# Kernel optimization log

Measured on AMD Instinct MI355X. Metric: run time of the kernel, lower is better.

## Reference

```python
import jax, jax.numpy as jnp
import numpy as np

N_SIDE = 8
N_PATCHES = 24
W_NORMALS = 1.0
W_PLANAR = 1.0
W_COLLISION = 0.01
W_TEMPLATE = 1.0
W_SYMMETRY = 0.0
SIGMA = 0.1

_lin = np.linspace(0.0, 1.0, N_SIDE).astype(np.float32)
_S, _T = np.meshgrid(_lin, _lin, indexing='ij')
S_GRID = jnp.asarray(_S.flatten())
T_GRID = jnp.asarray(_T.flatten())

def _build_topology():
    n = N_SIDE
    tris = []
    for i in range(n - 1):
        for j in range(n - 1):
            v00 = i * n + j; v10 = (i + 1) * n + j
            v01 = i * n + j + 1; v11 = (i + 1) * n + j + 1
            tris.append([v00, v10, v01]); tris.append([v10, v11, v01])
    tris = np.array(tris, dtype=np.int32)
    edges_pts = np.array([
        [i * n + 0 for i in range(n)],        # edge 0: t=0
        [(n - 1) * n + j for j in range(n)],  # edge 1: s=1
        [i * n + (n - 1) for i in range(n)],  # edge 2: t=1
        [0 * n + j for j in range(n)],        # edge 3: s=0
    ], dtype=np.int32)
    edges_tris = []
    for e in edges_pts:
        es = set(int(x) for x in e)
        et = [ti for ti, t in enumerate(tris) if len(es.intersection(int(v) for v in t)) >= 2]
        edges_tris.append(et[: n - 1])
    return tris, edges_pts, np.array(edges_tris, dtype=np.int32)

TRIANGULATION, GRID_POINT_EDGES, TRIANGULATION_EDGES = _build_topology()

ADJ_PAIRS = [(i, (i + 1) % N_PATCHES, 1) for i in range(N_PATCHES)]
_adjset = set(tuple(sorted((i, (i + 1) % N_PATCHES))) for i in range(N_PATCHES))
NONADJ_PAIRS = [(i, j) for i in range(N_PATCHES) for j in range(i + 1, N_PATCHES)
                if (i, j) not in _adjset]


def _bez_basis(u):
    return jnp.stack([(1 - u) ** 3, 3 * u * (1 - u) ** 2, 3 * u ** 2 * (1 - u), u ** 3], -1)


def coons_sample(s, t, patches):
    """patches [b,P,12,3] cubic-Bezier loop; returns [b,P,M,3]."""
    cp = patches
    c0 = cp[..., 0:4, :]
    c1 = cp[..., 3:7, :]
    c2 = cp[..., 6:10, :]
    c3 = jnp.concatenate([cp[..., 9:12, :], cp[..., 0:1, :]], axis=-2)
    cb = jnp.einsum('mk,bpkc->bpmc', _bez_basis(s), c0)
    cr = jnp.einsum('mk,bpkc->bpmc', _bez_basis(t), c1)
    ct = jnp.einsum('mk,bpkc->bpmc', _bez_basis(1 - s), c2)
    cl = jnp.einsum('mk,bpkc->bpmc', _bez_basis(1 - t), c3)
    P00 = cp[..., 0, :][:, :, None]; P10 = cp[..., 3, :][:, :, None]
    P11 = cp[..., 6, :][:, :, None]; P01 = cp[..., 9, :][:, :, None]
    s_ = s[None, None, :, None]; t_ = t[None, None, :, None]
    ruled = (1 - t_) * cb + t_ * ct + (1 - s_) * cl + s_ * cr
    bil = ((1 - s_) * (1 - t_) * P00 + s_ * (1 - t_) * P10
           + s_ * t_ * P11 + (1 - s_) * t_ * P01)
    return ruled - bil


def _pt_tri_sqdist(p, a, b, c):
    ab = b - a; ac = c - a; ap = p - a
    d1 = jnp.sum(ab * ap, -1); d2 = jnp.sum(ac * ap, -1)
    bp = p - b; d3 = jnp.sum(ab * bp, -1); d4 = jnp.sum(ac * bp, -1)
    cp = p - c; d5 = jnp.sum(ab * cp, -1); d6 = jnp.sum(ac * cp, -1)
    vc = d1 * d4 - d3 * d2; vb = d5 * d2 - d1 * d6; va = d3 * d6 - d5 * d4
    eps = 1e-12
    safe = lambda x: jnp.where(jnp.abs(x) < eps, eps, x)
    t_ab = jnp.clip(d1 / safe(d1 - d3), 0, 1)[..., None]
    t_ac = jnp.clip(d2 / safe(d2 - d6), 0, 1)[..., None]
    t_bc = jnp.clip((d4 - d3) / safe((d4 - d3) + (d5 - d6)), 0, 1)[..., None]
    denom = safe(va + vb + vc)
    v = (vb / denom)[..., None]; w = (vc / denom)[..., None]
    close = a + ab * v + ac * w
    close = jnp.where(((va <= 0) & ((d4 - d3) >= 0) & ((d5 - d6) >= 0))[..., None], b + (c - b) * t_bc, close)
    close = jnp.where(((vb <= 0) & (d2 >= 0) & (d6 <= 0))[..., None], a + ac * t_ac, close)
    close = jnp.where(((d6 >= 0) & (d5 <= d6))[..., None], c, close)
    close = jnp.where(((vc <= 0) & (d1 >= 0) & (d3 <= 0))[..., None], a + ab * t_ab, close)
    close = jnp.where(((d3 >= 0) & (d4 <= d3))[..., None], b, close)
    close = jnp.where(((d1 <= 0) & (d2 <= 0))[..., None], a, close)
    return jnp.sum((p - close) ** 2, -1)


def d_points_to_tris(points, tris):
    """points [K,P,3], tris [K,T,3,3] -> min distance per K."""
    p = points[:, :, None, :]
    a = tris[:, None, :, 0, :]; b = tris[:, None, :, 1, :]; c = tris[:, None, :, 2, :]
    d2 = _pt_tri_sqdist(p, a, b, c)  # [K,P,T]
    return jnp.sqrt(jnp.min(d2, axis=(1, 2)) + 1e-12)


def bboxes_intersect(p1, p2):
    """p1 [b,K,P,3], p2 [b,K,Q,3] -> [b,K] bool."""
    mn1 = p1.min(2); mx1 = p1.max(2); mn2 = p2.min(2); mx2 = p2.max(2)
    return jnp.all((mx1 >= mn2) & (mx2 >= mn1), -1)


def compute_chamfer_losses(points, normals, tp, tn):
    d = (jnp.sum(points ** 2, -1)[:, :, None] + jnp.sum(tp ** 2, -1)[:, None, :]
         - 2 * jnp.einsum('bnc,bmc->bnm', points, tp))
    ca = jnp.min(d, 2); ia = jnp.argmin(d, 2)
    cb = jnp.min(d, 1); ib = jnp.argmin(d, 1)
    na = jnp.sum((normals - jnp.take_along_axis(tn, ia[..., None], 1)) ** 2, -1)
    nb = jnp.sum((tn - jnp.take_along_axis(normals, ib[..., None], 1)) ** 2, -1)
    return ca, cb, na, nb


def planar_patch_loss(st, points, mtds):
    """st [M,2], points [b,P,M,3], mtds [b,P,M]: residual of best-fit linear map."""
    A = jnp.concatenate([st, jnp.ones_like(st[:, :1])], 1)  # [M,3]
    AtA = A.T @ A
    sol = jnp.linalg.solve(AtA, jnp.einsum('mk,bpmc->bpkc', A, points))
    res = points - jnp.einsum('mk,bpkc->bpmc', A, sol)
    l = jnp.sum(res ** 2, -1)
    return jnp.mean(jnp.sum(mtds * l, -1) / jnp.sum(mtds, -1))


def _gather2(x, idx):
    """x [b,K,N,...], idx [K,R] -> x gathered along axis 2."""
    full = idx.reshape((1,) + idx.shape + (1,) * (x.ndim - 3))
    full = jnp.broadcast_to(full, x.shape[:2] + (idx.shape[1],) + x.shape[3:])
    return jnp.take_along_axis(x, full, axis=2)


def _forward(target, patches, points, normals, mtds, st, template_normals):
    b, n_patches = patches.shape[0], patches.shape[1]
    target_points = target[:, :, :3]
    target_normals = target[:, :, 3:]
    pts_flat = points.reshape(b, -1, 3)
    nrm_flat = normals.reshape(b, -1, 3)
    mtds_flat = mtds.reshape(b, -1)

    ca, cb, na, nb = compute_chamfer_losses(pts_flat, nrm_flat, target_points, target_normals)
    ca = jnp.sum(mtds_flat * ca, -1) / jnp.sum(mtds_flat, -1)
    cb = cb.mean(1)
    chamfer_loss = ((ca + cb).mean() / 2).reshape(1)
    na = jnp.sum(mtds_flat * na, -1) / jnp.sum(mtds_flat, -1)
    nb = nb.mean(-1)
    normals_loss = ((na + nb).mean() / 2).reshape(1)

    tnl = jnp.sum((template_normals[None] - normals) ** 2, -1)  # [b,P,M]
    template_normals_loss = (jnp.sum(mtds * tnl, -1) / jnp.sum(mtds, -1)).mean().reshape(1)

    planar_loss = planar_patch_loss(st, points, mtds).reshape(1)

    # ---- collision ----
    tri_idx = jnp.asarray(TRIANGULATION)
    grid_points = coons_sample(S_GRID, T_GRID, patches)       # [b,P,64,3]
    triangles = grid_points[:, :, tri_idx]                    # [b,P,98,3,3]

    i1s, i2s, e1s = zip(*ADJ_PAIRS)
    i1s = np.array(i1s); i2s = np.array(i2s); e1s = np.array(e1s)
    K = len(e1s)
    pts1 = _gather2(grid_points[:, i1s], jnp.asarray(GRID_POINT_EDGES[e1s]))    # [b,K,8,3]
    tris1 = _gather2(triangles[:, i1s], jnp.asarray(TRIANGULATION_EDGES[e1s]))  # [b,K,7,3,3]
    pts2 = grid_points[:, i2s]
    tris2 = triangles[:, i2s]
    mask_adj = bboxes_intersect(pts1, pts2).any(0)  # [K]
    d1 = d_points_to_tris(pts1.reshape(b * K, 8, 3), tris2.reshape(b * K, -1, 3, 3))
    d2 = d_points_to_tris(pts2.reshape(b * K, -1, 3), tris1.reshape(b * K, -1, 3, 3))
    d = jnp.minimum(d1, d2).reshape(b, K)
    col_adj = jnp.where(mask_adj[None, :], jnp.exp(-(d / SIGMA) ** 2), 0.0)

    j1s, j2s = zip(*NONADJ_PAIRS)
    j1s = np.array(j1s); j2s = np.array(j2s)
    Kn = len(j1s)
    p1 = grid_points[:, j1s]; p2 = grid_points[:, j2s]
    t1 = triangles[:, j1s]; t2 = triangles[:, j2s]
    mask_non = bboxes_intersect(p1, p2).any(0)  # [Kn]
    d1 = d_points_to_tris(p1.reshape(b * Kn, -1, 3), t2.reshape(b * Kn, -1, 3, 3))
    d2 = d_points_to_tris(p2.reshape(b * Kn, -1, 3), t1.reshape(b * Kn, -1, 3, 3))
    dn = jnp.minimum(d1, d2).reshape(b, Kn)
    col_non = jnp.where(mask_non[None, :], jnp.exp(-(dn / SIGMA) ** 2), 0.0)

    collision_loss = (col_adj.sum(-1) + col_non.sum(-1)).mean().reshape(1)
    symmetry_loss = jnp.zeros(1, dtype=patches.dtype)

    loss = (chamfer_loss + W_NORMALS * normals_loss + W_COLLISION * collision_loss
            + W_PLANAR * planar_loss + W_TEMPLATE * template_normals_loss
            + W_SYMMETRY * symmetry_loss)
    return (loss, chamfer_loss, normals_loss, collision_loss, planar_loss,
            template_normals_loss, symmetry_loss)


def setup_inputs() -> dict:
    key = jax.random.key(0)
    ks = jax.random.split(key, 7)
    b, P, M, Mt = 4, N_PATCHES, 256, 4096
    return {
        'target': jax.random.normal(ks[0], (b, Mt, 6), jnp.float32),
        'patches': jax.random.normal(ks[1], (b, P, 12, 3), jnp.float32),
        'points': jax.random.normal(ks[2], (b, P, M, 3), jnp.float32),
        'normals': jax.random.normal(ks[3], (b, P, M, 3), jnp.float32),
        'mtds': jax.random.uniform(ks[4], (b, P, M), jnp.float32) + 0.01,
        'st': jax.random.uniform(ks[5], (M, 2), jnp.float32),
        'template_normals': jax.random.normal(ks[6], (P, M, 3), jnp.float32),
    }


def reference(target, patches, points, normals, mtds, st, template_normals):
    return _forward(target, patches, points, normals, mtds, st, template_normals)
```

## Files before the change

### kernel.cpp

```cpp
#include <hip/hip_runtime.h>
#include <math.h>

#define NPATCH 24
#define NB 4
#define MPTS 256
#define MT 4096
#define NPTS (NPATCH*MPTS)
#define GRIDPTS 64
#define SIGMA2INV 100.0f
#define PRUNE_MARGIN 0.45f


__device__ inline unsigned encodeFloat(float f) {
    unsigned u = __float_as_uint(f);
    return (u & 0x80000000u) ? ~u : (u | 0x80000000u);
}
__device__ inline float decodeFloat(unsigned e) {
    return __uint_as_float((e & 0x80000000u) ? (e ^ 0x80000000u) : ~e);
}

template<int NV>
__device__ inline void blockReduceSumN(const float* vals, float* out, float* scratch) {
    int wid = threadIdx.x >> 6, lane = threadIdx.x & 63;
#pragma unroll
    for (int i = 0; i < NV; ++i) {
        float v = vals[i];
        for (int o = 32; o > 0; o >>= 1) v += __shfl_down(v, o);
        if (lane == 0) scratch[wid * NV + i] = v;
    }
    __syncthreads();
    if (threadIdx.x < NV)
        out[threadIdx.x] = scratch[0 * NV + threadIdx.x] + scratch[1 * NV + threadIdx.x] +
                           scratch[2 * NV + threadIdx.x] + scratch[3 * NV + threadIdx.x];
    __syncthreads();
}

__device__ inline float clamp01f(float x) { return fminf(fmaxf(x, 0.0f), 1.0f); }
__device__ inline float safercp(float x) {
    float s = fabsf(x) < 1e-12f ? 1e-12f : x;
    return __builtin_amdgcn_rcpf(s);
}

__device__ inline float ptTriSqDistP(float px, float py, float pz, const float4* T) {
    float4 f0 = T[0], f1 = T[1], f2 = T[2], f3 = T[3];
    float ax = f0.x, ay = f0.y, az = f0.z;
    float abx = f1.x, aby = f1.y, abz = f1.z;
    float acx = f2.x, acy = f2.y, acz = f2.z;
    float abp = abx * px + aby * py + abz * pz;
    float acp = acx * px + acy * py + acz * pz;
    float d1 = abp - f0.w;
    float d2 = acp - f1.w;
    float d3 = abp - f2.w;
    float d4 = acp - f3.x;
    float d5 = abp - f3.y;
    float d6 = acp - f3.z;
    float vc = d1 * d4 - d3 * d2;
    float vb = d5 * d2 - d1 * d6;
    float va = d3 * d6 - d5 * d4;
    float t_ab = clamp01f(d1 * safercp(d1 - d3));
    float t_ac = clamp01f(d2 * safercp(d2 - d6));
    float t_bc = clamp01f((d4 - d3) * safercp((d4 - d3) + (d5 - d6)));
    float rden = safercp(va + vb + vc);
    float v = vb * rden, w = vc * rden;
    float clx = ax + abx * v + acx * w;
    float cly = ay + aby * v + acy * w;
    float clz = az + abz * v + acz * w;
    if (va <= 0.0f && (d4 - d3) >= 0.0f && (d5 - d6) >= 0.0f) {
        clx = (ax + abx) + (acx - abx) * t_bc;
        cly = (ay + aby) + (acy - aby) * t_bc;
        clz = (az + abz) + (acz - abz) * t_bc;
    }
    if (vb <= 0.0f && d2 >= 0.0f && d6 <= 0.0f) {
        clx = ax + acx * t_ac; cly = ay + acy * t_ac; clz = az + acz * t_ac;
    }
    if (d6 >= 0.0f && d5 <= d6) { clx = ax + acx; cly = ay + acy; clz = az + acz; }
    if (vc <= 0.0f && d1 >= 0.0f && d3 <= 0.0f) {
        clx = ax + abx * t_ab; cly = ay + aby * t_ab; clz = az + abz * t_ab;
    }
    if (d3 >= 0.0f && d4 <= d3) { clx = ax + abx; cly = ay + aby; clz = az + abz; }
    if (d1 <= 0.0f && d2 <= 0.0f) { clx = ax; cly = ay; clz = az; }
    float dx = px - clx, dy = py - cly, dz = pz - clz;
    return dx * dx + dy * dy + dz * dz;
}

__global__ __launch_bounds__(128) void k_coons_tri(const float* __restrict__ patches,
                                                   float* __restrict__ grid,
                                                   float* __restrict__ bbF,
                                                   float* __restrict__ bbE,
                                                   float4* __restrict__ TDg,
                                                   float4* __restrict__ TSg) {
    __shared__ float Pl[192];
    int bp = blockIdx.x;
    int m = threadIdx.x;
    if (m < 64) {
        int i = m >> 3, j = m & 7;
        float s = (i == 7) ? 1.0f : (float)i * (1.0f / 7.0f);
        float t = (j == 7) ? 1.0f : (float)j * (1.0f / 7.0f);
        const float* cp = patches + bp * 36;
        float bs[4], bt[4], bs1[4], bt1[4];
        {
            float u, vv;
            u = s; vv = 1.0f - u; bs[0] = vv * vv * vv; bs[1] = 3.f * u * vv * vv; bs[2] = 3.f * u * u * vv; bs[3] = u * u * u;
            u = t; vv = 1.0f - u; bt[0] = vv * vv * vv; bt[1] = 3.f * u * vv * vv; bt[2] = 3.f * u * u * vv; bt[3] = u * u * u;
            u = 1.0f - s; vv = 1.0f - u; bs1[0] = vv * vv * vv; bs1[1] = 3.f * u * vv * vv; bs1[2] = 3.f * u * u * vv; bs1[3] = u * u * u;
            u = 1.0f - t; vv = 1.0f - u; bt1[0] = vv * vv * vv; bt1[1] = 3.f * u * vv * vv; bt1[2] = 3.f * u * u * vv; bt1[3] = u * u * u;
        }
        float g[3];
#pragma unroll
        for (int c = 0; c < 3; ++c) {
            float cb = bs[0] * cp[0 * 3 + c] + bs[1] * cp[1 * 3 + c] + bs[2] * cp[2 * 3 + c] + bs[3] * cp[3 * 3 + c];
            float cr = bt[0] * cp[3 * 3 + c] + bt[1] * cp[4 * 3 + c] + bt[2] * cp[5 * 3 + c] + bt[3] * cp[6 * 3 + c];
            float ct = bs1[0] * cp[6 * 3 + c] + bs1[1] * cp[7 * 3 + c] + bs1[2] * cp[8 * 3 + c] + bs1[3] * cp[9 * 3 + c];
            float cl = bt1[0] * cp[9 * 3 + c] + bt1[1] * cp[10 * 3 + c] + bt1[2] * cp[11 * 3 + c] + bt1[3] * cp[0 * 3 + c];
            float P00 = cp[0 * 3 + c], P10 = cp[3 * 3 + c], P11 = cp[6 * 3 + c], P01 = cp[9 * 3 + c];
            float ruled = (1.0f - t) * cb + t * ct + (1.0f - s) * cl + s * cr;
            float bil = (1.0f - s) * (1.0f - t) * P00 + s * (1.0f - t) * P10 + s * t * P11 + (1.0f - s) * t * P01;
            g[c] = ruled - bil;
            grid[(bp * GRIDPTS + m) * 3 + c] = g[c];
            Pl[m * 3 + c] = g[c];
        }
        float mnF[3], mxF[3], mnE[3], mxE[3];
        bool edge = (m >= 56);
#pragma unroll
        for (int c = 0; c < 3; ++c) {
            mnF[c] = g[c]; mxF[c] = g[c];
            mnE[c] = edge ? g[c] : 1e30f;
            mxE[c] = edge ? g[c] : -1e30f;
        }
        for (int o = 32; o > 0; o >>= 1) {
#pragma unroll
            for (int c = 0; c < 3; ++c) {
                mnF[c] = fminf(mnF[c], __shfl_down(mnF[c], o));
                mxF[c] = fmaxf(mxF[c], __shfl_down(mxF[c], o));
                mnE[c] = fminf(mnE[c], __shfl_down(mnE[c], o));
                mxE[c] = fmaxf(mxE[c], __shfl_down(mxE[c], o));
            }
        }
        if (m == 0) {
#pragma unroll
            for (int c = 0; c < 3; ++c) {
                bbF[bp * 6 + c] = mnF[c]; bbF[bp * 6 + 3 + c] = mxF[c];
                bbE[bp * 6 + c] = mnE[c]; bbE[bp * 6 + 3 + c] = mxE[c];
            }
        }
    }
    __syncthreads();
    int t = m;
    if (t < 98) {
        int cell = t >> 1, ii = cell / 7, jj = cell - ii * 7;
        int v00 = ii * 8 + jj;
        int va, vb, vc;
        if (t & 1) { va = v00 + 8; vb = v00 + 9; vc = v00 + 1; }
        else       { va = v00;     vb = v00 + 8; vc = v00 + 1; }
        float ax = Pl[va * 3], ay = Pl[va * 3 + 1], az = Pl[va * 3 + 2];
        float bx = Pl[vb * 3], by = Pl[vb * 3 + 1], bz = Pl[vb * 3 + 2];
        float cx = Pl[vc * 3], cy = Pl[vc * 3 + 1], cz = Pl[vc * 3 + 2];
        float abx = bx - ax, aby = by - ay, abz = bz - az;
        float acx = cx - ax, acy = cy - ay, acz = cz - az;
        float ab_a = abx * ax + aby * ay + abz * az;
        float ac_a = acx * ax + acy * ay + acz * az;
        float ab_b = abx * bx + aby * by + abz * bz;
        float ac_b = acx * bx + acy * by + acz * bz;
        float ab_c = abx * cx + aby * cy + abz * cz;
        float ac_c = acx * cx + acy * cy + acz * cz;
        float4* dst = TDg + ((size_t)bp * 98 + t) * 4;
        dst[0] = make_float4(ax, ay, az, ab_a);
        dst[1] = make_float4(abx, aby, abz, ac_a);
        dst[2] = make_float4(acx, acy, acz, ab_b);
        dst[3] = make_float4(ac_b, ab_c, ac_c, 0.0f);
        float gx = (ax + bx + cx) * (1.0f / 3.0f);
        float gy = (ay + by + cy) * (1.0f / 3.0f);
        float gz = (az + bz + cz) * (1.0f / 3.0f);
        float ra = (ax - gx) * (ax - gx) + (ay - gy) * (ay - gy) + (az - gz) * (az - gz);
        float rb = (bx - gx) * (bx - gx) + (by - gy) * (by - gy) + (bz - gz) * (bz - gz);
        float rc = (cx - gx) * (cx - gx) + (cy - gy) * (cy - gy) + (cz - gz) * (cz - gz);
        float r = sqrtf(fmaxf(ra, fmaxf(rb, rc)));
        TSg[(size_t)bp * 98 + t] = make_float4(gx, gy, gz, r);
    }
}

__global__ __launch_bounds__(256) void k_mega(const float* __restrict__ target,
                                              const float* __restrict__ points,
                                              const float* __restrict__ grid,
                                              const float4* __restrict__ TDg,
                                              const float4* __restrict__ TSg,
                                              const float* __restrict__ bbF,
                                              const float* __restrict__ bbE,
                                              float* __restrict__ pa,
                                              float* __restrict__ pb,
                                              unsigned* __restrict__ pairmin) {
    __shared__ float4 smem[128];
    __shared__ float4 Pts[64];
    __shared__ float4 Sph[98];
    __shared__ unsigned short wl[6272];
    __shared__ int cnt;
    __shared__ float sred[4];
    int id = blockIdx.x;
    int b = blockIdx.y;
    int tid = threadIdx.x;

    if (id >= 528) {
        bool isA = (id < 624);
        int qbase, ch;
        float qx0, qy0, qz0, qx1, qy1, qz1, qx2, qy2, qz2, qx3, qy3, qz3;
        float qx4, qy4, qz4, qx5, qy5, qz5, qx6, qy6, qz6, qx7, qy7, qz7;
        if (isA) {
            int rel = id - 528;
            int qb = rel >> 5; ch = rel & 31;
            qbase = qb * 2048 + tid * 8;
            int chbase = ch * 128;
            if (tid < 128) {
                const float* tp = target + (size_t)(b * MT + chbase + tid) * 6;
                float x = tp[0], y = tp[1], z = tp[2];
                smem[tid] = make_float4(x, y, z, 0.5f * (x * x + y * y + z * z));
            }
            const float4* pf = (const float4*)(points + ((size_t)b * NPTS + qbase) * 3);
            float4 v0 = pf[0], v1 = pf[1], v2 = pf[2], v3 = pf[3], v4 = pf[4], v5 = pf[5];
            qx0 = v0.x; qy0 = v0.y; qz0 = v0.z;
            qx1 = v0.w; qy1 = v1.x; qz1 = v1.y;
            qx2 = v1.z; qy2 = v1.w; qz2 = v2.x;
            qx3 = v2.y; qy3 = v2.z; qz3 = v2.w;
            qx4 = v3.x; qy4 = v3.y; qz4 = v3.z;
            qx5 = v3.w; qy5 = v4.x; qz5 = v4.y;
            qx6 = v4.z; qy6 = v4.w; qz6 = v5.x;
            qx7 = v5.y; qy7 = v5.z; qz7 = v5.w;
        } else {
            int rel = id - 624;
            int qb = rel / 48; ch = rel - qb * 48;
            qbase = qb * 2048 + tid * 8;
            int chbase = ch * 128;
            if (tid < 128) {
                const float* pp = points + (size_t)(b * NPTS + chbase + tid) * 3;
                float x = pp[0], y = pp[1], z = pp[2];
                smem[tid] = make_float4(x, y, z, 0.5f * (x * x + y * y + z * z));
            }
            const float* tf = target + (size_t)(b * MT + qbase) * 6;
            float2 a0 = *(const float2*)(tf + 0);  float z0 = tf[2];
            float2 a1 = *(const float2*)(tf + 6);  float z1 = tf[8];
            float2 a2 = *(const float2*)(tf + 12); float z2 = tf[14];
            float2 a3 = *(const float2*)(tf + 18); float z3 = tf[20];
            float2 a4 = *(const float2*)(tf + 24); float z4 = tf[26];
            float2 a5 = *(const float2*)(tf + 30); float z5 = tf[32];
            float2 a6 = *(const float2*)(tf + 36); float z6 = tf[38];
            float2 a7 = *(const float2*)(tf + 42); float z7 = tf[44];
            qx0 = a0.x; qy0 = a0.y; qz0 = z0;
            qx1 = a1.x; qy1 = a1.y; qz1 = z1;
            qx2 = a2.x; qy2 = a2.y; qz2 = z2;
            qx3 = a3.x; qy3 = a3.y; qz3 = z3;
            qx4 = a4.x; qy4 = a4.y; qz4 = z4;
            qx5 = a5.x; qy5 = a5.y; qz5 = z5;
            qx6 = a6.x; qy6 = a6.y; qz6 = z6;
            qx7 = a7.x; qy7 = a7.y; qz7 = z7;
        }
        __syncthreads();
        float sc0 = 1e30f, sc1 = 1e30f, sc2 = 1e30f, sc3 = 1e30f;
        float sc4 = 1e30f, sc5 = 1e30f, sc6 = 1e30f, sc7 = 1e30f;
#pragma unroll 8
        for (int k = 0; k < 128; ++k) {
            float4 T = smem[k];
            sc0 = fminf(sc0, fmaf(-qx0, T.x, fmaf(-qy0, T.y, fmaf(-qz0, T.z, T.w))));
            sc1 = fminf(sc1, fmaf(-qx1, T.x, fmaf(-qy1, T.y, fmaf(-qz1, T.z, T.w))));
            sc2 = fminf(sc2, fmaf(-qx2, T.x, fmaf(-qy2, T.y, fmaf(-qz2, T.z, T.w))));
            sc3 = fminf(sc3, fmaf(-qx3, T.x, fmaf(-qy3, T.y, fmaf(-qz3, T.z, T.w))));
            sc4 = fminf(sc4, fmaf(-qx4, T.x, fmaf(-qy4, T.y, fmaf(-qz4, T.z, T.w))));
            sc5 = fminf(sc5, fmaf(-qx5, T.x, fmaf(-qy5, T.y, fmaf(-qz5, T.z, T.w))));
            sc6 = fminf(sc6, fmaf(-qx6, T.x, fmaf(-qy6, T.y, fmaf(-qz6, T.z, T.w))));
            sc7 = fminf(sc7, fmaf(-qx7, T.x, fmaf(-qy7, T.y, fmaf(-qz7, T.z, T.w))));
        }
        float* dstp = isA ? (pa + ((size_t)(b * 32 + ch)) * NPTS + qbase)
                          : (pb + ((size_t)(b * 48 + ch)) * MT + qbase);
        *(float4*)(dstp) = make_float4(sc0, sc1, sc2, sc3);
        *(float4*)(dstp + 4) = make_float4(sc4, sc5, sc6, sc7);
        return;
    }

    float best = 1e30f;
    int pairIdx;

    if (id < 24) {
        int pair = id;
        pairIdx = pair;
        int i1 = pair, i2 = (pair + 1) % NPATCH;
        bool mask = false;
        for (int bb = 0; bb < NB; ++bb) {
            const float* B1 = bbE + (bb * NPATCH + i1) * 6;
            const float* B2 = bbF + (bb * NPATCH + i2) * 6;
            bool it = (B1[3] >= B2[0]) && (B2[3] >= B1[0]) &&
                      (B1[4] >= B2[1]) && (B2[4] >= B1[1]) &&
                      (B1[5] >= B2[2]) && (B2[5] >= B1[2]);
            mask |= it;
        }
        if (!mask) return;
        const float* P1 = grid + (size_t)(b * NPATCH + i1) * 192;
        const float* P2 = grid + (size_t)(b * NPATCH + i2) * 192;
        const float4* T1 = TDg + (size_t)(b * NPATCH + i1) * 98 * 4;
        const float4* T2 = TDg + (size_t)(b * NPATCH + i2) * 98 * 4;
        for (int tt = tid; tt < 1232; tt += 256) {
            const float4* T;
            float px, py, pz;
            if (tt < 784) {
                int ptI = tt / 98, tri = tt - ptI * 98;
                const float* gp = P1 + (56 + ptI) * 3;
                px = gp[0]; py = gp[1]; pz = gp[2];
                T = T2 + tri * 4;
            } else {
                int rr = tt - 784;
                int ptI = rr / 7, e = rr - ptI * 7;
                const float* gp = P2 + ptI * 3;
                px = gp[0]; py = gp[1]; pz = gp[2];
                T = T1 + (85 + 2 * e) * 4;
            }
            best = fminf(best, ptTriSqDistP(px, py, pz, T));
        }
    } else {
        int r = id - 24;
        int pi2 = r >> 1, dir = r & 1;
        pairIdx = 24 + pi2;
        int k = pi2, i1 = 0;
        while (i1 < NPATCH) {
            int cnt_ = (i1 == 0) ? 21 : (22 - i1);
            if (k < cnt_) break;
            k -= cnt_; ++i1;
        }
        int i2 = i1 + 2 + k;
        bool mask = false;
        for (int bb = 0; bb < NB; ++bb) {
            const float* B1 = bbF + (bb * NPATCH + i1) * 6;
            const float* B2 = bbF + (bb * NPATCH + i2) * 6;
            bool it = (B1[3] >= B2[0]) && (B2[3] >= B1[0]) &&
                      (B1[4] >= B2[1]) && (B2[4] >= B1[1]) &&
                      (B1[5] >= B2[2]) && (B2[5] >= B1[2]);
            mask |= it;
        }
        if (!mask) return;
        int ip_pts = dir ? i2 : i1;
        int ip_tri = dir ? i1 : i2;
        if (tid < 64) {
            const float* gp = grid + ((size_t)(b * NPATCH + ip_pts) * 64 + tid) * 3;
            Pts[tid] = make_float4(gp[0], gp[1], gp[2], 0.0f);
        } else if (tid < 128) {
            int q = tid - 64;
            const float* gq = grid + ((size_t)(b * NPATCH + ip_tri) * 64 + q) * 3;
            smem[q] = make_float4(gq[0], gq[1], gq[2], 0.0f);
        } else if (tid < 226) {
            int t = tid - 128;
            Sph[t] = TSg[(size_t)(b * NPATCH + ip_tri) * 98 + t];
        }
        if (tid == 0) cnt = 0;
        __syncthreads();
        int pt = tid & 63;
        float4 P = Pts[pt];
        float px = P.x, py = P.y, pz = P.z;
        float ub = 1e30f;
        int o0 = (tid >> 6) * 16;
        for (int q = o0; q < o0 + 16; ++q) {
            float4 Q = smem[q];
            float dx = px - Q.x, dy = py - Q.y, dz = pz - Q.z;
            ub = fminf(ub, dx * dx + dy * dy + dz * dz);
        }
        for (int o = 32; o > 0; o >>= 1) ub = fminf(ub, __shfl_xor(ub, o));
        if ((tid & 63) == 0) sred[tid >> 6] = ub;
        __syncthreads();
        ub = fminf(fminf(sred[0], sred[1]), fminf(sred[2], sred[3]));
        float sB = fminf(sqrtf(ub) + 1e-4f, PRUNE_MARGIN);
        best = ub;
        int wtri = tid >> 6;
        for (int t = wtri; t < 98; t += 4) {
            float4 S = Sph[t];
            float dx = px - S.x, dy = py - S.y, dz = pz - S.z;
            float lb = dx * dx + dy * dy + dz * dz;
            float thr = sB + S.w;
            if (lb <= thr * thr) {
                int idx = atomicAdd(&cnt, 1);
                wl[idx] = (unsigned short)((pt << 7) | t);
            }
        }
        __syncthreads();
        int n = cnt;
        const float4* TD = TDg + (size_t)(b * NPATCH + ip_tri) * 98 * 4;
        for (int i = tid; i < n; i += 256) {
            int w = wl[i];
            int ppt = w >> 7, t = w & 127;
            float4 PP = Pts[ppt];
            best = fminf(best, ptTriSqDistP(PP.x, PP.y, PP.z, TD + t * 4));
        }
        __syncthreads();
    }

    for (int o = 32; o > 0; o >>= 1) best = fminf(best, __shfl_down(best, o));
    if ((tid & 63) == 0) sred[tid >> 6] = best;
    __syncthreads();
    if (tid == 0) {
        float d2 = fminf(fminf(sred[0], sred[1]), fminf(sred[2], sred[3]));
        atomicMin(&pairmin[b * 276 + pairIdx], encodeFloat(d2));
    }
}

__global__ __launch_bounds__(256) void k_final(const float* __restrict__ points,
                                               const float* __restrict__ normals,
                                               const float* __restrict__ target,
                                               const float* __restrict__ mtds,
                                               const float* __restrict__ st,
                                               const float* __restrict__ tmpl,
                                               const float* __restrict__ pa,
                                               const float* __restrict__ pb,
                                               float* __restrict__ acc) {
    int id = blockIdx.x, b = blockIdx.y;
    if (id < 24) {
        int p = id;
        int m = threadIdx.x;
        int bp = b * NPATCH + p;
        const float* pp = points + (size_t)(bp * MPTS + m) * 3;
        float px = pp[0], py = pp[1], pz = pp[2];
        float pn = px * px + py * py + pz * pz;
        const float* nr = normals + (size_t)(bp * MPTS + m) * 3;
        float nx = nr[0], ny = nr[1], nz = nr[2];
        float w = mtds[bp * MPTS + m];
        float s = st[2 * m], t = st[2 * m + 1];

        int q = p * MPTS + m;
        const float* paB = pa + (size_t)b * 32 * NPTS;
        float minv = 1e30f; int minch = 0;
#pragma unroll
        for (int ch = 0; ch < 32; ++ch) {
            float v = paB[ch * NPTS + q];
            if (v < minv) { minv = v; minch = ch; }
        }
        int base = minch * 128;
        const float* tb0 = target + (size_t)b * MT * 6;
        float smin = 1e30f; int ia = 0;
        for (int k = 0; k < 128; ++k) {
            const float* tq2 = tb0 + (size_t)(base + k) * 6;
            float x = tq2[0], yv = tq2[1], zv = tq2[2];
            float hw = 0.5f * (x * x + yv * yv + zv * zv);
            float sv = fmaf(-px, x, fmaf(-py, yv, fmaf(-pz, zv, hw)));
            if (sv < smin) { smin = sv; ia = base + k; }
        }
        float ca = fmaf(2.0f, smin, pn);
        const float* tq = tb0 + (size_t)ia * 6 + 3;
        float dx = nx - tq[0], dy = ny - tq[1], dz = nz - tq[2];
        float na = dx * dx + dy * dy + dz * dz;
        const float* tm = tmpl + (size_t)(p * MPTS + m) * 3;
        float ex = tm[0] - nx, ey = tm[1] - ny, ez = tm[2] - nz;
        float tnl = ex * ex + ey * ey + ez * ez;

        float vals[18];
        vals[0] = w * ca; vals[1] = w * na; vals[2] = w; vals[3] = w * tnl;
        vals[4] = s * px; vals[5] = s * py; vals[6] = s * pz;
        vals[7] = t * px; vals[8] = t * py; vals[9] = t * pz;
        vals[10] = px; vals[11] = py; vals[12] = pz;
        vals[13] = s * s; vals[14] = s * t; vals[15] = s; vals[16] = t * t; vals[17] = t;

        __shared__ float scratch[4 * 18];
        __shared__ float red[18];
        blockReduceSumN<18>(vals, red, scratch);

        __shared__ float sol[9];
        __shared__ float smtd_sh;
        if (threadIdx.x == 0) {
            float a00 = red[13], a01 = red[14], a02 = red[15];
            float a11 = red[16], a12 = red[17], a22 = 256.0f;
            float c00 = a11 * a22 - a12 * a12;
            float c01 = a02 * a12 - a01 * a22;
            float c02 = a01 * a12 - a02 * a11;
            float det = a00 * c00 + a01 * c01 + a02 * c02;
            float idet = 1.0f / det;
            float i00 = c00 * idet, i01 = c01 * idet, i02 = c02 * idet;
            float i11 = (a00 * a22 - a02 * a02) * idet;
            float i12 = (a01 * a02 - a00 * a12) * idet;
            float i22 = (a00 * a11 - a01 * a01) * idet;
#pragma unroll
            for (int c = 0; c < 3; ++c) {
                float b0 = red[4 + c], b1 = red[7 + c], b2 = red[10 + c];
                sol[0 * 3 + c] = i00 * b0 + i01 * b1 + i02 * b2;
                sol[1 * 3 + c] = i01 * b0 + i11 * b1 + i12 * b2;
                sol[2 * 3 + c] = i02 * b0 + i12 * b1 + i22 * b2;
            }
            smtd_sh = red[2];
            atomicAdd(&acc[0 + b], red[0]);
            atomicAdd(&acc[4 + b], red[1]);
            atomicAdd(&acc[8 + b], red[2]);
            atomicAdd(&acc[20], red[3] / red[2]);
        }
        __syncthreads();
        float rx = px - (s * sol[0] + t * sol[3] + sol[6]);
        float ry = py - (s * sol[1] + t * sol[4] + sol[7]);
        float rz = pz - (s * sol[2] + t * sol[5] + sol[8]);
        float v2 = w * (rx * rx + ry * ry + rz * rz);
        for (int o = 32; o > 0; o >>= 1) v2 += __shfl_down(v2, o);
        __shared__ float s2[4];
        if ((threadIdx.x & 63) == 0) s2[threadIdx.x >> 6] = v2;
        __syncthreads();
        if (threadIdx.x == 0)
            atomicAdd(&acc[21], (s2[0] + s2[1] + s2[2] + s2[3]) / smtd_sh);
    } else {
        int mc = id - 24;
        int mt = mc * 256 + threadIdx.x;
        const float* tq = target + (size_t)(b * MT + mt) * 6;
        float tx = tq[0], ty = tq[1], tz = tq[2];
        float tn2 = tx * tx + ty * ty + tz * tz;

        const float* pbB = pb + (size_t)b * 48 * MT;
        float minv = 1e30f; int minch = 0;
#pragma unroll
        for (int ch = 0; ch < 48; ++ch) {
            float v = pbB[ch * MT + mt];
            if (v < minv) { minv = v; minch = ch; }
        }
        int base = minch * 128;
        const float* pt0 = points + (size_t)b * NPTS * 3;
        float smin = 1e30f; int ib = 0;
        for (int k = 0; k < 128; ++k) {
            const float* pp2 = pt0 + (size_t)(base + k) * 3;
            float x = pp2[0], yv = pp2[1], zv = pp2[2];
            float hw = 0.5f * (x * x + yv * yv + zv * zv);
            float sv = fmaf(-tx, x, fmaf(-ty, yv, fmaf(-tz, zv, hw)));
            if (sv < smin) { smin = sv; ib = base + k; }
        }
        float cb = fmaf(2.0f, smin, tn2);
        const float* nr = normals + (size_t)(b * NPTS + ib) * 3;
        float dx = tq[3] - nr[0], dy = tq[4] - nr[1], dz = tq[5] - nr[2];
        float nb = dx * dx + dy * dy + dz * dz;
        float vals[2] = {cb, nb};
        __shared__ float scratchB[4 * 2];
        __shared__ float redB[2];
        blockReduceSumN<2>(vals, redB, scratchB);
        if (threadIdx.x == 0) {
            atomicAdd(&acc[12 + b], redB[0]);
            atomicAdd(&acc[16 + b], redB[1]);
        }
    }
}

__global__ __launch_bounds__(256) void k_finish(const float* __restrict__ acc,
                                                const unsigned* __restrict__ pairmin,
                                                float* __restrict__ out) {
    int tid = threadIdx.x;
    float s = 0.0f;
    for (int idx = tid; idx < 4 * 276; idx += 256) {
        unsigned key = pairmin[idx];
        if (key != 0xFFFFFFFFu) {
            float d2 = decodeFloat(key);
            s += expf(-(d2 + 1e-12f) * SIGMA2INV);
        }
    }
    for (int o = 32; o > 0; o >>= 1) s += __shfl_down(s, o);
    __shared__ float sred[4];
    if ((tid & 63) == 0) sred[tid >> 6] = s;
    __syncthreads();
    if (tid == 0) {
        float col = (sred[0] + sred[1] + sred[2] + sred[3]) * 0.25f;
        float ch = 0.0f, no = 0.0f;
        for (int b = 0; b < NB; ++b) {
            float caw = acc[0 + b] / acc[8 + b];
            float naw = acc[4 + b] / acc[8 + b];
            float cbm = acc[12 + b] / (float)MT;
            float nbm = acc[16 + b] / (float)MT;
            ch += caw + cbm;
            no += naw + nbm;
        }
        ch = ch * 0.25f * 0.5f;
        no = no * 0.25f * 0.5f;
        float tpl = acc[20] / 96.0f;
        float pl = acc[21] / 96.0f;
        float loss = ch + no + 0.01f * col + pl + tpl;
        out[0] = loss;
        out[1] = ch;
        out[2] = no;
        out[3] = col;
        out[4] = pl;
        out[5] = tpl;
        out[6] = 0.0f;
    }
}

extern "C" void kernel_launch(void* const* d_in, const int* in_sizes, int n_in,
                              void* d_out, int out_size, void* d_ws, size_t ws_size,
                              hipStream_t stream) {
    (void)in_sizes; (void)n_in; (void)out_size; (void)ws_size;
    const float* target = (const float*)d_in[0];
    const float* patches = (const float*)d_in[1];
    const float* points = (const float*)d_in[2];
    const float* normals = (const float*)d_in[3];
    const float* mtds = (const float*)d_in[4];
    const float* st = (const float*)d_in[5];
    const float* tmpl = (const float*)d_in[6];
    float* out = (float*)d_out;
    char* ws = (char*)d_ws;

    float* grid = (float*)(ws + 0);
    float* bbF = (float*)(ws + 73728);
    float* bbE = (float*)(ws + 76032);
    unsigned* pairmin = (unsigned*)(ws + 78336);
    float* acc = (float*)(ws + 82752);
    float4* TDg = (float4*)(ws + 82880);
    float4* TSg = (float4*)(ws + 684992);
    float* pa = (float*)(ws + 835520);
    float* pb = (float*)(ws + 3981248);

    hipMemsetAsync(ws + 78336, 0xFF, 4416, stream);
    hipMemsetAsync(ws + 82752, 0, 128, stream);

    k_coons_tri<<<dim3(NB * NPATCH), dim3(128), 0, stream>>>(patches, grid, bbF, bbE, TDg, TSg);
    k_mega<<<dim3(720, NB), dim3(256), 0, stream>>>(target, points, grid, TDg, TSg,
                                                    bbF, bbE, pa, pb, pairmin);
    k_final<<<dim3(40, NB), dim3(256), 0, stream>>>(points, normals, target, mtds, st,
                                                    tmpl, pa, pb, acc);
    k_finish<<<1, 256, 0, stream>>>(acc, pairmin, out);
}
```

Before: 78.18 us.

## Split chamfer argmin into wave-per-point kernel, fold memsets, ballot-aggregate worklist

Moves the per-point chunk argmin and 128-candidate nearest-neighbour search out of k_final into a new kernel that assigns one 64-lane wave per query point. Each wave reduces a packed (distance,index) 64-bit key with shuffles, and the result goes to workspace for k_final to decode. The two hipMemsetAsync calls are replaced by initialisation inside k_coons_tri block 0. The collision worklist append now uses one wave-level ballot and a single atomicAdd per wave instead of one atomic per thread. This removes a serial 128-iteration loop per thread and some launch overhead, at the cost of an extra kernel launch and an extra global round trip for the keys.

```diff
diff --git a/kernel.cpp b/kernel.cpp
--- a/kernel.cpp
+++ b/kernel.cpp
@@ -17,6 +17,14 @@
 }
 __device__ inline float decodeFloat(unsigned e) {
     return __uint_as_float((e & 0x80000000u) ? (e ^ 0x80000000u) : ~e);
+}
+
+__device__ inline unsigned long long waveMinU64(unsigned long long k) {
+    for (int o = 32; o > 0; o >>= 1) {
+        unsigned long long other = __shfl_xor(k, o);
+        k = (other < k) ? other : k;
+    }
+    return k;
 }
 
 template<int NV>
@@ -88,10 +96,16 @@
                                                    float* __restrict__ bbF,
                                                    float* __restrict__ bbE,
                                                    float4* __restrict__ TDg,
-                                                   float4* __restrict__ TSg) {
+                                                   float4* __restrict__ TSg,
+                                                   unsigned* __restrict__ pairmin,
+                                                   float* __restrict__ acc) {
     __shared__ float Pl[192];
     int bp = blockIdx.x;
     int m = threadIdx.x;
+    if (bp == 0) {
+        for (int i = m; i < 1104; i += 128) pairmin[i] = 0xFFFFFFFFu;
+        if (m < 32) acc[m] = 0.0f;
+    }
     if (m < 64) {
         int i = m >> 3, j = m & 7;
         float s = (i == 7) ? 1.0f : (float)i * (1.0f / 7.0f);
@@ -364,15 +378,23 @@
         ub = fminf(fminf(sred[0], sred[1]), fminf(sred[2], sred[3]));
         float sB = fminf(sqrtf(ub) + 1e-4f, PRUNE_MARGIN);
         best = ub;
+        int lane = tid & 63;
         int wtri = tid >> 6;
         for (int t = wtri; t < 98; t += 4) {
             float4 S = Sph[t];
             float dx = px - S.x, dy = py - S.y, dz = pz - S.z;
             float lb = dx * dx + dy * dy + dz * dz;
             float thr = sB + S.w;
-            if (lb <= thr * thr) {
-                int idx = atomicAdd(&cnt, 1);
-                wl[idx] = (unsigned short)((pt << 7) | t);
+            bool pred = (lb <= thr * thr);
+            unsigned long long mb = __ballot(pred);
+            if (mb != 0ull) {
+                int wbase;
+                if (lane == 0) wbase = atomicAdd(&cnt, __popcll(mb));
+                wbase = __shfl(wbase, 0);
+                if (pred) {
+                    int off = __popcll(mb & ((1ull << lane) - 1ull));
+                    wl[wbase + off] = (unsigned short)((pt << 7) | t);
+                }
             }
         }
         __syncthreads();
@@ -396,14 +418,72 @@
     }
 }
 
+__global__ __launch_bounds__(256) void k_argmin(const float* __restrict__ target,
+                                                const float* __restrict__ points,
+                                                const float* __restrict__ pa,
+                                                const float* __restrict__ pb,
+                                                unsigned long long* __restrict__ best_a,
+                                                unsigned long long* __restrict__ best_b) {
+    int w = blockIdx.x * 4 + (threadIdx.x >> 6);
+    int lane = threadIdx.x & 63;
+    if (w < 24576) {
+        int b = w / NPTS, qi = w - b * NPTS;
+        float v = (lane < 32) ? pa[((size_t)(b * 32 + lane)) * NPTS + qi] : 1e30f;
+        unsigned long long key = ((unsigned long long)encodeFloat(v) << 32) | (unsigned)lane;
+        key = waveMinU64(key);
+        int minch = (int)(key & 0xffffffffu);
+        int base = minch * 128;
+        const float* pp = points + ((size_t)b * NPTS + qi) * 3;
+        float px = pp[0], py = pp[1], pz = pp[2];
+        const float* tb0 = target + (size_t)b * MT * 6;
+        unsigned long long bk = 0xFFFFFFFFFFFFFFFFull;
+#pragma unroll
+        for (int rr = 0; rr < 2; ++rr) {
+            int k = base + lane + rr * 64;
+            const float* tq = tb0 + (size_t)k * 6;
+            float x = tq[0], y = tq[1], z = tq[2];
+            float hw = 0.5f * (x * x + y * y + z * z);
+            float s = fmaf(-px, x, fmaf(-py, y, fmaf(-pz, z, hw)));
+            unsigned long long kk = ((unsigned long long)encodeFloat(s) << 32) | (unsigned)k;
+            bk = (kk < bk) ? kk : bk;
+        }
+        bk = waveMinU64(bk);
+        if (lane == 0) best_a[(size_t)b * NPTS + qi] = bk;
+    } else {
+        int idx = w - 24576;
+        int b = idx / MT, mt = idx - b * MT;
+        float v = (lane < 48) ? pb[((size_t)(b * 48 + lane)) * MT + mt] : 1e30f;
+        unsigned long long key = ((unsigned long long)encodeFloat(v) << 32) | (unsigned)lane;
+        key = waveMinU64(key);
+        int minch = (int)(key & 0xffffffffu);
+        int base = minch * 128;
+        const float* tq = target + (size_t)(b * MT + mt) * 6;
+        float tx = tq[0], ty = tq[1], tz = tq[2];
+        const float* pt0 = points + (size_t)b * NPTS * 3;
+        unsigned long long bk = 0xFFFFFFFFFFFFFFFFull;
+#pragma unroll
+        for (int rr = 0; rr < 2; ++rr) {
+            int k = base + lane + rr * 64;
+            const float* pp2 = pt0 + (size_t)k * 3;
+            float x = pp2[0], y = pp2[1], z = pp2[2];
+            float hw = 0.5f * (x * x + y * y + z * z);
+            float s = fmaf(-tx, x, fmaf(-ty, y, fmaf(-tz, z, hw)));
+            unsigned long long kk = ((unsigned long long)encodeFloat(s) << 32) | (unsigned)k;
+            bk = (kk < bk) ? kk : bk;
+        }
+        bk = waveMinU64(bk);
+        if (lane == 0) best_b[(size_t)b * MT + mt] = bk;
+    }
+}
+
 __global__ __launch_bounds__(256) void k_final(const float* __restrict__ points,
                                                const float* __restrict__ normals,
                                                const float* __restrict__ target,
                                                const float* __restrict__ mtds,
                                                const float* __restrict__ st,
                                                const float* __restrict__ tmpl,
-                                               const float* __restrict__ pa,
-                                               const float* __restrict__ pb,
+                                               const unsigned long long* __restrict__ best_a,
+                                               const unsigned long long* __restrict__ best_b,
                                                float* __restrict__ acc) {
     int id = blockIdx.x, b = blockIdx.y;
     if (id < 24) {
@@ -417,27 +497,10 @@
         float nx = nr[0], ny = nr[1], nz = nr[2];
         float w = mtds[bp * MPTS + m];
         float s = st[2 * m], t = st[2 * m + 1];
-
-        int q = p * MPTS + m;
-        const float* paB = pa + (size_t)b * 32 * NPTS;
-        float minv = 1e30f; int minch = 0;
-#pragma unroll
-        for (int ch = 0; ch < 32; ++ch) {
-            float v = paB[ch * NPTS + q];
-            if (v < minv) { minv = v; minch = ch; }
-        }
-        int base = minch * 128;
-        const float* tb0 = target + (size_t)b * MT * 6;
-        float smin = 1e30f; int ia = 0;
-        for (int k = 0; k < 128; ++k) {
-            const float* tq2 = tb0 + (size_t)(base + k) * 6;
-            float x = tq2[0], yv = tq2[1], zv = tq2[2];
-            float hw = 0.5f * (x * x + yv * yv + zv * zv);
-            float sv = fmaf(-px, x, fmaf(-py, yv, fmaf(-pz, zv, hw)));
-            if (sv < smin) { smin = sv; ia = base + k; }
-        }
-        float ca = fmaf(2.0f, smin, pn);
-        const float* tq = tb0 + (size_t)ia * 6 + 3;
+        unsigned long long pk = best_a[(size_t)b * NPTS + p * MPTS + m];
+        float ca = fmaf(2.0f, decodeFloat((unsigned)(pk >> 32)), pn);
+        int ia = (int)(pk & 0xffffffffu);
+        const float* tq = target + (size_t)(b * MT + ia) * 6 + 3;
         float dx = nx - tq[0], dy = ny - tq[1], dz = nz - tq[2];
         float na = dx * dx + dy * dy + dz * dz;
         const float* tm = tmpl + (size_t)(p * MPTS + m) * 3;
@@ -499,25 +562,9 @@
         const float* tq = target + (size_t)(b * MT + mt) * 6;
         float tx = tq[0], ty = tq[1], tz = tq[2];
         float tn2 = tx * tx + ty * ty + tz * tz;
-
-        const float* pbB = pb + (size_t)b * 48 * MT;
-        float minv = 1e30f; int minch = 0;
-#pragma unroll
-        for (int ch = 0; ch < 48; ++ch) {
-            float v = pbB[ch * MT + mt];
-            if (v < minv) { minv = v; minch = ch; }
-        }
-        int base = minch * 128;
-        const float* pt0 = points + (size_t)b * NPTS * 3;
-        float smin = 1e30f; int ib = 0;
-        for (int k = 0; k < 128; ++k) {
-            const float* pp2 = pt0 + (size_t)(base + k) * 3;
-            float x = pp2[0], yv = pp2[1], zv = pp2[2];
-            float hw = 0.5f * (x * x + yv * yv + zv * zv);
-            float sv = fmaf(-tx, x, fmaf(-ty, yv, fmaf(-tz, zv, hw)));
-            if (sv < smin) { smin = sv; ib = base + k; }
-        }
-        float cb = fmaf(2.0f, smin, tn2);
+        unsigned long long pk = best_b[(size_t)b * MT + mt];
+        float cb = fmaf(2.0f, decodeFloat((unsigned)(pk >> 32)), tn2);
+        int ib = (int)(pk & 0xffffffffu);
         const float* nr = normals + (size_t)(b * NPTS + ib) * 3;
         float dx = tq[3] - nr[0], dy = tq[4] - nr[1], dz = tq[5] - nr[2];
         float nb = dx * dx + dy * dy + dz * dz;
@@ -597,14 +644,15 @@
     float4* TSg = (float4*)(ws + 684992);
     float* pa = (float*)(ws + 835520);
     float* pb = (float*)(ws + 3981248);
-
-    hipMemsetAsync(ws + 78336, 0xFF, 4416, stream);
-    hipMemsetAsync(ws + 82752, 0, 128, stream);
-
-    k_coons_tri<<<dim3(NB * NPATCH), dim3(128), 0, stream>>>(patches, grid, bbF, bbE, TDg, TSg);
+    unsigned long long* best_a = (unsigned long long*)(ws + 7126976);
+    unsigned long long* best_b = (unsigned long long*)(ws + 7323584);
+
+    k_coons_tri<<<dim3(NB * NPATCH), dim3(128), 0, stream>>>(patches, grid, bbF, bbE,
+                                                             TDg, TSg, pairmin, acc);
     k_mega<<<dim3(720, NB), dim3(256), 0, stream>>>(target, points, grid, TDg, TSg,
                                                     bbF, bbE, pa, pb, pairmin);
+    k_argmin<<<dim3(10240), dim3(256), 0, stream>>>(target, points, pa, pb, best_a, best_b);
     k_final<<<dim3(40, NB), dim3(256), 0, stream>>>(points, normals, target, mtds, st,
-                                                    tmpl, pa, pb, acc);
+                                                    tmpl, best_a, best_b, acc);
     k_finish<<<1, 256, 0, stream>>>(acc, pairmin, out);
 }
```

After: 75.32 us. 3.7% less time.
